# Optimization experiments

Hardware: AMD Instinct MI355X
Metric: run time of the kernel (lower is better)

## Reference

```python
import jax, jax.numpy as jnp
import numpy as np

E = 192      # embed_dim
DI = 384     # d_inner = 2*E (mamba default expand=2)
S = 16       # d_state
R = 12       # dt_rank = ceil(E/16)
DEPTH = 4
STRIDE = 4
P = 400      # num_patches = 1600/4
NC = 20
BATCH = 32
EPS = 1e-5


def _rmsnorm(x, w):
    x = x.astype(jnp.float32)
    return x * jax.lax.rsqrt(jnp.mean(x * x, axis=-1, keepdims=True) + EPS) * w


def _mamba_mixer(h, in_w, cw, cb, xpw, dtw, dtb, a_log, d_skip, ow):
    # h: [B, L, E]
    Bsz, Ln, _ = h.shape
    xz = jnp.einsum('ble,de->bld', h, in_w)            # [B,L,2*DI]
    xm, z = xz[..., :DI], xz[..., DI:]
    # causal depthwise conv1d, kernel 4 (left pad 3, truncate to L)
    xp = jnp.pad(xm, ((0, 0), (3, 0), (0, 0)))
    xc = sum(xp[:, k:k + Ln, :] * cw[:, k] for k in range(4)) + cb
    xc = jax.nn.silu(xc)
    xdb = jnp.einsum('bld,rd->blr', xc, xpw)           # [B,L,R+2S]
    dt = jax.nn.softplus(jnp.einsum('blr,dr->bld', xdb[..., :R], dtw) + dtb)
    Bm = xdb[..., R:R + S]
    Cm = xdb[..., R + S:]
    A = -jnp.exp(a_log)                                # [DI,S]

    def step(hst, inp):
        dt_t, b_t, c_t, u_t = inp                      # [B,DI],[B,S],[B,S],[B,DI]
        dA = jnp.exp(dt_t[:, :, None] * A)             # [B,DI,S]
        hst = dA * hst + (dt_t * u_t)[:, :, None] * b_t[:, None, :]
        y_t = jnp.einsum('bdn,bn->bd', hst, c_t)
        return hst, y_t

    h0 = jnp.zeros((Bsz, DI, S), xc.dtype)
    xs = (dt.transpose(1, 0, 2), Bm.transpose(1, 0, 2), Cm.transpose(1, 0, 2), xc.transpose(1, 0, 2))
    _, ys = jax.lax.scan(step, h0, xs)
    y = ys.transpose(1, 0, 2) + xc * d_skip
    y = y * jax.nn.silu(z)
    return jnp.einsum('bld,ed->ble', y, ow)


def _forward(imgs, patch_w, patch_b, cls_token, pos_embed, cnn_w, cnn_b, norm_w,
             in_proj_w, conv_w, conv_b, x_proj_w, dt_proj_w, dt_proj_b, A_log, D,
             out_proj_w, norm_f_w, head_w, head_b):
    Bsz = imgs.shape[0]
    # StrideEmbed: conv1d kernel=stride=4 == reshape + matmul
    x = imgs.reshape(Bsz, P, STRIDE)
    x = jnp.einsum('blk,ek->ble', x, patch_w[:, 0, :]) + patch_b   # [B,P,E]
    x = x + pos_embed[:, :-1, :]
    # depthwise conv1d k=3 pad=1 over length
    xp = jnp.pad(x, ((0, 0), (1, 1), (0, 0)))
    x = sum(xp[:, k:k + P, :] * cnn_w[:, 0, k] for k in range(3)) + cnn_b
    cls = cls_token + pos_embed[:, -1, :]                           # [1,1,E]
    x = jnp.concatenate([x, jnp.broadcast_to(cls, (Bsz, 1, E))], axis=1)  # [B,401,E]

    hidden = x
    residual = None
    for i in range(DEPTH):
        residual = hidden if residual is None else residual + hidden
        hn = _rmsnorm(residual, norm_w[i])
        hidden = _mamba_mixer(hn, in_proj_w[i], conv_w[i], conv_b[i], x_proj_w[i],
                              dt_proj_w[i], dt_proj_b[i], A_log[i], D[i], out_proj_w[i])
    out = _rmsnorm(hidden + residual, norm_f_w)
    v_sem = out[:, -1, :]
    return v_sem @ head_w.T + head_b


def setup_inputs() -> dict:
    key = jax.random.key(0)
    ks = jax.random.split(key, 12)
    n = lambda k, shp, s=0.02: jax.random.normal(k, shp, dtype=jnp.float32) * s
    return {
        'imgs': jax.random.normal(ks[0], (BATCH, 1, 40, 40), jnp.float32),
        'patch_w': n(ks[1], (E, 1, STRIDE), 0.3),
        'patch_b': jnp.zeros((E,), jnp.float32),
        'cls_token': n(ks[2], (1, 1, E)),
        'pos_embed': n(ks[3], (1, P + 1, E)),
        'cnn_w': n(ks[4], (E, 1, 3), 0.3),
        'cnn_b': jnp.zeros((E,), jnp.float32),
        'norm_w': jnp.ones((DEPTH, E), jnp.float32),
        'in_proj_w': n(ks[5], (DEPTH, 2 * DI, E), 0.05),
        'conv_w': n(ks[6], (DEPTH, DI, 4), 0.3),
        'conv_b': jnp.zeros((DEPTH, DI), jnp.float32),
        'x_proj_w': n(ks[7], (DEPTH, R + 2 * S, DI), 0.05),
        'dt_proj_w': n(ks[8], (DEPTH, DI, R), 0.3),
        'dt_proj_b': jnp.log(jnp.expm1(jax.random.uniform(ks[9], (DEPTH, DI), minval=0.001, maxval=0.1))),
        'A_log': jnp.log(jnp.broadcast_to(jnp.arange(1, S + 1, dtype=jnp.float32), (DEPTH, DI, S))),
        'D': jnp.ones((DEPTH, DI), jnp.float32),
        'out_proj_w': n(ks[10], (DEPTH, E, DI), 0.05),
        'norm_f_w': jnp.ones((E,), jnp.float32),
        'head_w': n(ks[11], (NC, E)),
        'head_b': jnp.zeros((NC,), jnp.float32),
    }


def reference(imgs, patch_w, patch_b, cls_token, pos_embed, cnn_w, cnn_b, norm_w,
              in_proj_w, conv_w, conv_b, x_proj_w, dt_proj_w, dt_proj_b, A_log, D,
              out_proj_w, norm_f_w, head_w, head_b):
    return _forward(imgs, patch_w, patch_b, cls_token, pos_embed, cnn_w, cnn_b, norm_w,
                    in_proj_w, conv_w, conv_b, x_proj_w, dt_proj_w, dt_proj_b, A_log, D,
                    out_proj_w, norm_f_w, head_w, head_b)
```

## Files before the change

kernel.cpp:

```cpp
#include <hip/hip_runtime.h>
#include <math.h>

#define E 192
#define DI 384
#define S 16
#define R 12
#define DEPTH 4
#define P 400
#define NC 20
#define BATCH 32
#define L 401
#define NTOK (BATCH * L)
#define CH 32
#define NCH 13

using short8 = __attribute__((ext_vector_type(8))) short;
using float4v = __attribute__((ext_vector_type(4))) float;

__device__ __forceinline__ float siluf(float x) {
    return x / (1.f + __expf(-x));
}
__device__ __forceinline__ float softplusf(float x) {
    return (x > 20.f) ? x : log1pf(__expf(x));
}
__device__ __forceinline__ unsigned short f2bf(float x) {
    unsigned int u = __float_as_uint(x);
    unsigned int r = 0x7fffu + ((u >> 16) & 1u);
    return (unsigned short)((u + r) >> 16);
}
__device__ __forceinline__ float bf2f(unsigned short v) {
    return __uint_as_float(((unsigned int)v) << 16);
}

__global__ void k_embed(const float* __restrict__ imgs, const float* __restrict__ patch_w,
                        const float* __restrict__ patch_b, const float* __restrict__ cls_token,
                        const float* __restrict__ pos_embed, const float* __restrict__ cnn_w,
                        const float* __restrict__ cnn_b, float* __restrict__ resid) {
    int idx = blockIdx.x * blockDim.x + threadIdx.x;
    if (idx >= NTOK * E) return;
    int e = idx % E;
    int bl = idx / E;
    int l = bl % L;
    int b = bl / L;
    float out;
    if (l == P) {
        out = cls_token[e] + pos_embed[(size_t)P * E + e];
    } else {
        float w0 = patch_w[e * 4 + 0], w1 = patch_w[e * 4 + 1];
        float w2 = patch_w[e * 4 + 2], w3 = patch_w[e * 4 + 3];
        float pb = patch_b[e];
        const float* ib = imgs + (size_t)b * 1600;
        auto xe = [&](int ll) -> float {
            const float* ip = ib + ll * 4;
            return ip[0] * w0 + ip[1] * w1 + ip[2] * w2 + ip[3] * w3 + pb +
                   pos_embed[(size_t)ll * E + e];
        };
        float c0 = cnn_w[e * 3 + 0], c1 = cnn_w[e * 3 + 1], c2 = cnn_w[e * 3 + 2];
        float acc = cnn_b[e] + xe(l) * c1;
        if (l > 0) acc += xe(l - 1) * c0;
        if (l < P - 1) acc += xe(l + 1) * c2;
        out = acc;
    }
    resid[idx] = out;
}

__global__ void k_rmsnorm(const float* __restrict__ resid, unsigned short* __restrict__ hn,
                          const float* __restrict__ w) {
    int wave = blockIdx.x * (blockDim.x >> 6) + (threadIdx.x >> 6);
    int lane = threadIdx.x & 63;
    if (wave >= NTOK) return;
    size_t base = (size_t)wave * E;
    float v[3];
    float ss = 0.f;
#pragma unroll
    for (int j = 0; j < 3; j++) {
        int e = lane + j * 64;
        float r = resid[base + e];
        v[j] = r;
        ss += r * r;
    }
#pragma unroll
    for (int off = 32; off > 0; off >>= 1) ss += __shfl_xor(ss, off, 64);
    float scale = rsqrtf(ss * (1.f / (float)E) + 1e-5f);
#pragma unroll
    for (int j = 0; j < 3; j++) {
        int e = lane + j * 64;
        hn[base + e] = f2bf(v[j] * scale * w[e]);
    }
}

__global__ void k_prep(const float* __restrict__ in_proj_w, const float* __restrict__ x_proj_w,
                       const float* __restrict__ out_proj_w, const float* __restrict__ A_log,
                       const float* __restrict__ dt_proj_w,
                       unsigned short* __restrict__ w_in, unsigned short* __restrict__ w_x,
                       unsigned short* __restrict__ w_out, float* __restrict__ negA,
                       float* __restrict__ dtw_t) {
    const int n1 = DEPTH * 2 * DI * E;
    const int n2 = DEPTH * 44 * DI;
    const int n3 = DEPTH * E * DI;
    const int n4 = DEPTH * DI * S;
    const int n5 = DEPTH * DI * R;
    int idx = blockIdx.x * blockDim.x + threadIdx.x;
    if (idx < n1) {
        w_in[idx] = f2bf(in_proj_w[idx]);
    } else if (idx < n1 + n2) {
        int i = idx - n1;
        w_x[i] = f2bf(x_proj_w[i]);
    } else if (idx < n1 + n2 + n3) {
        int i = idx - n1 - n2;
        w_out[i] = f2bf(out_proj_w[i]);
    } else if (idx < n1 + n2 + n3 + n4) {
        int i = idx - n1 - n2 - n3;
        int layer = i / (DI * S);
        int rem = i % (DI * S);
        int n = rem / DI;
        int d = rem % DI;
        negA[i] = -__expf(A_log[(size_t)layer * DI * S + d * S + n]);
    } else if (idx < n1 + n2 + n3 + n4 + n5) {
        int i = idx - n1 - n2 - n3 - n4;
        int layer = i / (DI * R);
        int rem = i % (DI * R);
        int r = rem / DI;
        int d = rem % DI;
        dtw_t[i] = dt_proj_w[(size_t)layer * DI * R + d * R + r];
    }
}

__global__ void k_flag(const float* __restrict__ negA, int* __restrict__ flag) {
    int idx = blockIdx.x * blockDim.x + threadIdx.x;
    if (idx >= DEPTH * DI) return;
    int layer = idx / DI;
    int d = idx % DI;
    const float* base = negA + (size_t)layer * DI * S;
    float a0 = base[d];
    bool ok = true;
#pragma unroll
    for (int n = 1; n < S; n++) {
        float an = base[n * DI + d];
        ok = ok && (fabsf(an - (float)(n + 1) * a0) <= 1e-5f * fabsf(an));
    }
    flag[idx] = ok ? 1 : 0;
}

template <int BM, int BN, int EPI>
__global__ __launch_bounds__(256) void k_gemm_bf16(const unsigned short* __restrict__ A,
                                                   const unsigned short* __restrict__ W,
                                                   float* __restrict__ C,
                                                   unsigned short* __restrict__ XM,
                                                   unsigned short* __restrict__ Z,
                                                   int M, int N, int K) {
    constexpr int BK = 64, PADK = BK + 8;
    constexpr int MT = BM / 32, NT = BN / 32;
    __shared__ unsigned short As[BM][PADK];
    __shared__ unsigned short Bs[BN][PADK];
    int tid = threadIdx.x;
    int m0 = blockIdx.y * BM, n0 = blockIdx.x * BN;
    int wave = tid >> 6, lane = tid & 63;
    int row16 = lane & 15, quad = lane >> 4;
    int wm0 = (wave >> 1) * (BM / 2), wn0 = (wave & 1) * (BN / 2);

    float4v acc[MT][NT];
#pragma unroll
    for (int i = 0; i < MT; i++)
#pragma unroll
        for (int j = 0; j < NT; j++) acc[i][j] = (float4v){0.f, 0.f, 0.f, 0.f};

    for (int k0 = 0; k0 < K; k0 += BK) {
#pragma unroll
        for (int p = 0; p < MT; p++) {
            int idx = (p * 256 + tid) * 8;
            int row = idx / BK, col = idx % BK;
            int gm = m0 + row;
            short8 v;
            if (gm < M)
                v = *(const short8*)&A[(size_t)gm * K + k0 + col];
            else
                v = (short8)0;
            *(short8*)&As[row][col] = v;
        }
#pragma unroll
        for (int p = 0; p < NT; p++) {
            int idx = (p * 256 + tid) * 8;
            int row = idx / BK, col = idx % BK;
            int gn = n0 + row;
            short8 v;
            if (gn < N)
                v = *(const short8*)&W[(size_t)gn * K + k0 + col];
            else
                v = (short8)0;
            *(short8*)&Bs[row][col] = v;
        }
        __syncthreads();
#pragma unroll
        for (int kk = 0; kk < BK; kk += 32) {
            int koff = kk + quad * 8;
            short8 af[MT], bfr[NT];
#pragma unroll
            for (int i = 0; i < MT; i++)
                af[i] = *(const short8*)&As[wm0 + i * 16 + row16][koff];
#pragma unroll
            for (int j = 0; j < NT; j++)
                bfr[j] = *(const short8*)&Bs[wn0 + j * 16 + row16][koff];
#pragma unroll
            for (int i = 0; i < MT; i++)
#pragma unroll
                for (int j = 0; j < NT; j++)
                    acc[i][j] = __builtin_amdgcn_mfma_f32_16x16x32_bf16(af[i], bfr[j],
                                                                        acc[i][j], 0, 0, 0);
        }
        __syncthreads();
    }
#pragma unroll
    for (int i = 0; i < MT; i++) {
#pragma unroll
        for (int j = 0; j < NT; j++) {
#pragma unroll
            for (int r = 0; r < 4; r++) {
                int m = m0 + wm0 + i * 16 + quad * 4 + r;
                int n = n0 + wn0 + j * 16 + row16;
                if (m >= M || n >= N) continue;
                float v = acc[i][j][r];
                if (EPI == 0) {
                    C[(size_t)m * N + n] = v;
                } else if (EPI == 1) {
                    if (n < DI)
                        XM[(size_t)m * DI + n] = f2bf(v);
                    else
                        Z[(size_t)m * DI + (n - DI)] = f2bf(v);
                } else {
                    C[(size_t)m * N + n] += v;
                }
            }
        }
    }
}

__global__ void k_conv(const unsigned short* __restrict__ xm_bf, const float* __restrict__ cw,
                       const float* __restrict__ cb, unsigned short* __restrict__ xc_bf) {
    int idx = blockIdx.x * blockDim.x + threadIdx.x;
    if (idx >= NTOK * DI) return;
    int d = idx % DI;
    int bl = idx / DI;
    int l = bl % L;
    int b = bl / L;
    const unsigned short* base = xm_bf + (size_t)b * L * DI + d;
    float acc = cb[d];
#pragma unroll
    for (int k = 0; k < 4; k++) {
        int ll = l - 3 + k;
        if (ll >= 0) acc += bf2f(base[(size_t)ll * DI]) * cw[d * 4 + k];
    }
    xc_bf[idx] = f2bf(siluf(acc));
}

__global__ __launch_bounds__(384) void k_dtpre(
        const float* __restrict__ xdb, const float* __restrict__ dtw_t,
        const float* __restrict__ dtb, float* __restrict__ dtbuf) {
    int tok = blockIdx.x;
    int d = threadIdx.x;
    const float* xr = xdb + (size_t)tok * 44;
    float acc = dtb[d];
#pragma unroll
    for (int r = 0; r < R; r++) acc += xr[r] * dtw_t[r * DI + d];
    dtbuf[(size_t)tok * DI + d] = softplusf(acc);
}

template <bool LAST>
__global__ __launch_bounds__(384) void k_scanA(
        const unsigned short* __restrict__ xc_bf, const float* __restrict__ xdb,
        const float* __restrict__ dtbuf, const float* __restrict__ negA_l,
        const int* __restrict__ flag_l, const float* __restrict__ Dskip,
        float2* __restrict__ ydt, float* __restrict__ hend) {
    int d = threadIdx.x;
    int ch = blockIdx.x;
    int b = blockIdx.y;
    int t0 = ch * CH;
    int t1 = min(t0 + CH, L);
    bool fast = __all(flag_l[d] != 0);
    float a0 = negA_l[d];
    float a[S];
    if (!fast) {
#pragma unroll
        for (int n = 0; n < S; n++) a[n] = negA_l[n * DI + d];
    }
    float dsk = Dskip[d];
    float h[S] = {};
    float dts = 0.f;
    size_t tok0 = (size_t)b * L + t0;
    float dt_nx = dtbuf[tok0 * DI + d];
    float u_nx = bf2f(xc_bf[tok0 * DI + d]);
    float e1_nx = __expf(a0 * dt_nx);
    for (int t = t0; t < t1; t++) {
        size_t tok = (size_t)b * L + t;
        float dtv = dt_nx, e1v = e1_nx, uu = u_nx;
        if (t + 1 < t1) {
            dt_nx = dtbuf[(tok + 1) * DI + d];
            u_nx = bf2f(xc_bf[(tok + 1) * DI + d]);
            e1_nx = __expf(a0 * dt_nx);
        }
        const float* row = xdb + tok * 44;
        dts += dtv;
        float dtu = dtv * uu;
        float y = uu * dsk;
        if (fast) {
            float p = e1v;
#pragma unroll
            for (int n = 0; n < S; n++) {
                h[n] = p * h[n] + dtu * row[R + n];
                y += h[n] * row[R + S + n];
                p *= e1v;
            }
        } else {
#pragma unroll
            for (int n = 0; n < S; n++) {
                float dA = __expf(dtv * a[n]);
                h[n] = dA * h[n] + dtu * row[R + n];
                y += h[n] * row[R + S + n];
            }
        }
        if (!LAST || t == P || t == t1 - 1) ydt[tok * DI + d] = make_float2(y, dts);
    }
    float* he = hend + ((size_t)(b * NCH + ch) * S) * DI + d;
#pragma unroll
    for (int n = 0; n < S; n++) he[n * DI] = h[n];
}

__global__ void k_scanB(const float* __restrict__ hend, const float2* __restrict__ ydt,
                        const float* __restrict__ negA_l, const int* __restrict__ flag_l,
                        float* __restrict__ hinit) {
    int idx = blockIdx.x * blockDim.x + threadIdx.x;
    if (idx >= BATCH * DI) return;
    int d = idx % DI;
    int b = idx / DI;
    bool fast = __all(flag_l[d] != 0);
    float a[S];
#pragma unroll
    for (int n = 0; n < S; n++) a[n] = negA_l[n * DI + d];
    float h[S] = {};
    for (int ch = 0; ch < NCH; ch++) {
        size_t o = ((size_t)(b * NCH + ch) * S) * DI + d;
#pragma unroll
        for (int n = 0; n < S; n++) hinit[o + n * DI] = h[n];
        int tlast = min(ch * CH + CH, L) - 1;
        float dts = ydt[((size_t)b * L + tlast) * DI + d].y;
        if (fast) {
            float e1c = __expf(a[0] * dts);
            float p = e1c;
#pragma unroll
            for (int n = 0; n < S; n++) {
                h[n] = p * h[n] + hend[o + n * DI];
                p *= e1c;
            }
        } else {
#pragma unroll
            for (int n = 0; n < S; n++) h[n] = __expf(dts * a[n]) * h[n] + hend[o + n * DI];
        }
    }
}

__global__ __launch_bounds__(384) void k_fixup(
        const unsigned short* __restrict__ z_bf, const float* __restrict__ xdb,
        const float* __restrict__ negA_l, const int* __restrict__ flag_l,
        const float* __restrict__ hinit, const float2* __restrict__ ydt,
        unsigned short* __restrict__ y_bf) {
    int tok = blockIdx.x;
    int d = threadIdx.x;
    int l = tok % L;
    int b = tok / L;
    int ch = l / CH;
    size_t idx = (size_t)tok * DI + d;
    float2 yd = ydt[idx];
    float y = yd.x;
    if (ch != 0) {
        bool fast = __all(flag_l[d] != 0);
        const float* h0 = hinit + ((size_t)(b * NCH + ch) * S) * DI + d;
        const float* cv = xdb + (size_t)tok * 44 + R + S;
        float dts = yd.y;
        float corr = 0.f;
        if (fast) {
            float e1c = __expf(negA_l[d] * dts);
            float p = e1c;
#pragma unroll
            for (int n = 0; n < S; n++) {
                corr += cv[n] * p * h0[n * DI];
                p *= e1c;
            }
        } else {
#pragma unroll
            for (int n = 0; n < S; n++)
                corr += cv[n] * __expf(negA_l[n * DI + d] * dts) * h0[n * DI];
        }
        y += corr;
    }
    float z = bf2f(z_bf[idx]);
    y_bf[idx] = f2bf(y * siluf(z));
}

__global__ __launch_bounds__(384) void k_fixup_last(
        const unsigned short* __restrict__ z_bf, const float* __restrict__ xdb,
        const float* __restrict__ negA_l, const int* __restrict__ flag_l,
        const float* __restrict__ hinit, const float2* __restrict__ ydt,
        unsigned short* __restrict__ y32) {
    int b = blockIdx.x;
    int d = threadIdx.x;
    int tok = b * L + P;
    int ch = P / CH;
    size_t idx = (size_t)tok * DI + d;
    float2 yd = ydt[idx];
    float y = yd.x;
    {
        bool fast = __all(flag_l[d] != 0);
        const float* h0 = hinit + ((size_t)(b * NCH + ch) * S) * DI + d;
        const float* cv = xdb + (size_t)tok * 44 + R + S;
        float dts = yd.y;
        float corr = 0.f;
        if (fast) {
            float e1c = __expf(negA_l[d] * dts);
            float p = e1c;
#pragma unroll
            for (int n = 0; n < S; n++) {
                corr += cv[n] * p * h0[n * DI];
                p *= e1c;
            }
        } else {
#pragma unroll
            for (int n = 0; n < S; n++)
                corr += cv[n] * __expf(negA_l[n * DI + d] * dts) * h0[n * DI];
        }
        y += corr;
    }
    float z = bf2f(z_bf[idx]);
    y32[(size_t)b * DI + d] = f2bf(y * siluf(z));
}

__global__ void k_head(const float* __restrict__ resid, const float* __restrict__ hidden32,
                       const float* __restrict__ norm_f_w, const float* __restrict__ head_w,
                       const float* __restrict__ head_b, float* __restrict__ out) {
    __shared__ float v[E];
    int b = blockIdx.x;
    int lane = threadIdx.x;
    size_t base = ((size_t)b * L + P) * E;
    float loc[3];
    float ss = 0.f;
#pragma unroll
    for (int j = 0; j < 3; j++) {
        int e = lane + j * 64;
        float x = resid[base + e] + hidden32[(size_t)b * E + e];
        loc[j] = x;
        ss += x * x;
    }
#pragma unroll
    for (int off = 32; off > 0; off >>= 1) ss += __shfl_xor(ss, off, 64);
    float scale = rsqrtf(ss * (1.f / (float)E) + 1e-5f);
#pragma unroll
    for (int j = 0; j < 3; j++) {
        int e = lane + j * 64;
        v[e] = loc[j] * scale * norm_f_w[e];
    }
    __syncthreads();
    if (lane < NC) {
        float acc = head_b[lane];
        for (int e = 0; e < E; e++) acc += v[e] * head_w[lane * E + e];
        out[b * NC + lane] = acc;
    }
}

extern "C" void kernel_launch(void* const* d_in, const int* in_sizes, int n_in,
                              void* d_out, int out_size, void* d_ws, size_t ws_size,
                              hipStream_t stream) {
    const float* imgs      = (const float*)d_in[0];
    const float* patch_w   = (const float*)d_in[1];
    const float* patch_b   = (const float*)d_in[2];
    const float* cls_token = (const float*)d_in[3];
    const float* pos_embed = (const float*)d_in[4];
    const float* cnn_w     = (const float*)d_in[5];
    const float* cnn_b     = (const float*)d_in[6];
    const float* norm_w    = (const float*)d_in[7];
    const float* in_proj_w = (const float*)d_in[8];
    const float* conv_w    = (const float*)d_in[9];
    const float* conv_b    = (const float*)d_in[10];
    const float* x_proj_w  = (const float*)d_in[11];
    const float* dt_proj_w = (const float*)d_in[12];
    const float* dt_proj_b = (const float*)d_in[13];
    const float* A_log     = (const float*)d_in[14];
    const float* Dskip     = (const float*)d_in[15];
    const float* out_proj_w= (const float*)d_in[16];
    const float* norm_f_w  = (const float*)d_in[17];
    const float* head_w    = (const float*)d_in[18];
    const float* head_b    = (const float*)d_in[19];

    float* ws = (float*)d_ws;
    size_t off = 0;
    float* resid  = ws + off; off += (size_t)NTOK * E;
    float* xdb    = ws + off; off += (size_t)NTOK * 44;
    float* dtbuf  = ws + off; off += (size_t)NTOK * DI;
    float* ydt    = ws + off; off += (size_t)NTOK * DI * 2;
    float* hend   = ws + off; off += (size_t)BATCH * NCH * DI * S;
    float* hinit  = ws + off; off += (size_t)BATCH * NCH * DI * S;
    float* negA   = ws + off; off += (size_t)DEPTH * DI * S;
    float* dtw_t  = ws + off; off += (size_t)DEPTH * DI * R;
    float* hid32  = ws + off; off += (size_t)BATCH * E;
    int*   gflag  = (int*)(ws + off); off += (size_t)DEPTH * DI;
    unsigned short* xm_bf  = (unsigned short*)(ws + off); off += (size_t)NTOK * DI / 2;
    unsigned short* z_bf   = (unsigned short*)(ws + off); off += (size_t)NTOK * DI / 2;
    unsigned short* bf_buf = (unsigned short*)(ws + off); off += (size_t)NTOK * DI / 2;
    unsigned short* y32_bf = (unsigned short*)(ws + off); off += (size_t)BATCH * DI / 2 + 16;
    unsigned short* w_in  = (unsigned short*)(ws + off); off += (size_t)DEPTH * 2 * DI * E / 2;
    unsigned short* w_x   = (unsigned short*)(ws + off); off += (size_t)DEPTH * 44 * DI / 2 + 16;
    unsigned short* w_out = (unsigned short*)(ws + off); off += (size_t)DEPTH * E * DI / 2;

    unsigned short* hn_bf = bf_buf;
    unsigned short* xc_bf = bf_buf;
    unsigned short* y_bf  = bf_buf;

    {
        int ntot = DEPTH * (2 * DI * E + 44 * DI + E * DI + DI * S + DI * R);
        k_prep<<<(ntot + 255) / 256, 256, 0, stream>>>(in_proj_w, x_proj_w, out_proj_w, A_log,
                                                       dt_proj_w, w_in, w_x, w_out, negA,
                                                       dtw_t);
        k_flag<<<(DEPTH * DI + 255) / 256, 256, 0, stream>>>(negA, gflag);
    }

    k_embed<<<(NTOK * E) / 256, 256, 0, stream>>>(imgs, patch_w, patch_b, cls_token,
                                                  pos_embed, cnn_w, cnn_b, resid);

    for (int i = 0; i < DEPTH; i++) {
        k_rmsnorm<<<NTOK / 4, 256, 0, stream>>>(resid, hn_bf, norm_w + i * E);

        {
            dim3 g((2 * DI) / 64, (NTOK + 127) / 128);
            k_gemm_bf16<128, 64, 1><<<g, 256, 0, stream>>>(
                hn_bf, w_in + (size_t)i * 2 * DI * E, nullptr, xm_bf, z_bf, NTOK, 2 * DI, E);
        }
        k_conv<<<(NTOK * DI) / 256, 256, 0, stream>>>(xm_bf, conv_w + (size_t)i * DI * 4,
                                                      conv_b + (size_t)i * DI, xc_bf);
        {
            dim3 g(1, NTOK / 32);
            k_gemm_bf16<32, 64, 0><<<g, 256, 0, stream>>>(
                xc_bf, w_x + (size_t)i * 44 * DI, xdb, nullptr, nullptr, NTOK, 44, DI);
        }
        const float* nA = negA + (size_t)i * DI * S;
        const int* fl = gflag + (size_t)i * DI;
        k_dtpre<<<NTOK, 384, 0, stream>>>(xdb, dtw_t + (size_t)i * DI * R,
                                          dt_proj_b + (size_t)i * DI, dtbuf);
        dim3 g(NCH, BATCH);
        if (i < DEPTH - 1) {
            k_scanA<false><<<g, DI, 0, stream>>>(xc_bf, xdb, dtbuf, nA, fl,
                                                 Dskip + (size_t)i * DI, (float2*)ydt, hend);
            k_scanB<<<(BATCH * DI + 255) / 256, 256, 0, stream>>>(hend, (const float2*)ydt,
                                                                  nA, fl, hinit);
            k_fixup<<<NTOK, 384, 0, stream>>>(z_bf, xdb, nA, fl, hinit,
                                              (const float2*)ydt, y_bf);
            dim3 go(E / 64, (NTOK + 63) / 64);
            k_gemm_bf16<64, 64, 2><<<go, 256, 0, stream>>>(
                y_bf, w_out + (size_t)i * E * DI, resid, nullptr, nullptr, NTOK, E, DI);
        } else {
            k_scanA<true><<<g, DI, 0, stream>>>(xc_bf, xdb, dtbuf, nA, fl,
                                                Dskip + (size_t)i * DI, (float2*)ydt, hend);
            k_scanB<<<(BATCH * DI + 255) / 256, 256, 0, stream>>>(hend, (const float2*)ydt,
                                                                  nA, fl, hinit);
            k_fixup_last<<<BATCH, 384, 0, stream>>>(z_bf, xdb, nA, fl, hinit,
                                                    (const float2*)ydt, y32_bf);
            dim3 go(E / 64, 1);
            k_gemm_bf16<32, 64, 0><<<go, 256, 0, stream>>>(
                y32_bf, w_out + (size_t)i * E * DI, hid32, nullptr, nullptr, BATCH, E, DI);
        }
    }

    k_head<<<BATCH, 64, 0, stream>>>(resid, hid32, norm_f_w, head_w, head_b, (float*)d_out);
}
```

Measured before the change: 731.1 us.

## Fuse causal depthwise conv into x_proj GEMM and retile in/out projections

Removes the standalone depthwise conv kernel and computes conv+SiLU while loading A tiles in a new x_proj GEMM kernel, still writing xc_bf for the scan. This saves one launch and a separate read of xm plus the reread of xc. The in_proj GEMM tile grows to 128x128 and the out_proj GEMM tile to 128x64. The trade-offs are that each xm element is loaded four times inside the fused kernel, and the larger tiles give fewer blocks per launch.

```diff
diff --git a/kernel.cpp b/kernel.cpp
--- a/kernel.cpp
+++ b/kernel.cpp
@@ -235,22 +235,100 @@
     }
 }
 
-__global__ void k_conv(const unsigned short* __restrict__ xm_bf, const float* __restrict__ cw,
-                       const float* __restrict__ cb, unsigned short* __restrict__ xc_bf) {
-    int idx = blockIdx.x * blockDim.x + threadIdx.x;
-    if (idx >= NTOK * DI) return;
-    int d = idx % DI;
-    int bl = idx / DI;
-    int l = bl % L;
-    int b = bl / L;
-    const unsigned short* base = xm_bf + (size_t)b * L * DI + d;
-    float acc = cb[d];
-#pragma unroll
-    for (int k = 0; k < 4; k++) {
-        int ll = l - 3 + k;
-        if (ll >= 0) acc += bf2f(base[(size_t)ll * DI]) * cw[d * 4 + k];
-    }
-    xc_bf[idx] = f2bf(siluf(acc));
+template <int BM, int BN>
+__global__ __launch_bounds__(256) void k_xproj_conv(
+        const unsigned short* __restrict__ xm, const unsigned short* __restrict__ W,
+        const float* __restrict__ cw, const float* __restrict__ cb,
+        float* __restrict__ C, unsigned short* __restrict__ xc_bf, int M, int N) {
+    constexpr int K = DI, BK = 64, PADK = BK + 8;
+    constexpr int MT = BM / 32, NT = BN / 32;
+    __shared__ unsigned short As[BM][PADK];
+    __shared__ unsigned short Bs[BN][PADK];
+    int tid = threadIdx.x;
+    int m0 = blockIdx.y * BM;
+    int wave = tid >> 6, lane = tid & 63;
+    int row16 = lane & 15, quad = lane >> 4;
+    int wm0 = (wave >> 1) * (BM / 2), wn0 = (wave & 1) * (BN / 2);
+
+    float4v acc[MT][NT];
+#pragma unroll
+    for (int i = 0; i < MT; i++)
+#pragma unroll
+        for (int j = 0; j < NT; j++) acc[i][j] = (float4v){0.f, 0.f, 0.f, 0.f};
+
+    for (int k0 = 0; k0 < K; k0 += BK) {
+#pragma unroll
+        for (int p = 0; p < MT; p++) {
+            int idx = (p * 256 + tid) * 8;
+            int row = idx / BK, col = idx % BK;
+            int t = m0 + row;
+            short8 v = (short8)0;
+            if (t < M) {
+                int l = t % L;
+                int d0 = k0 + col;
+                float av[8];
+#pragma unroll
+                for (int j = 0; j < 8; j++) av[j] = cb[d0 + j];
+#pragma unroll
+                for (int k = 0; k < 4; k++) {
+                    int ll = l - 3 + k;
+                    if (ll >= 0) {
+                        short8 xv = *(const short8*)&xm[(size_t)(t - 3 + k) * DI + d0];
+#pragma unroll
+                        for (int j = 0; j < 8; j++)
+                            av[j] += bf2f((unsigned short)xv[j]) * cw[(d0 + j) * 4 + k];
+                    }
+                }
+#pragma unroll
+                for (int j = 0; j < 8; j++) v[j] = (short)f2bf(siluf(av[j]));
+                *(short8*)&xc_bf[(size_t)t * DI + d0] = v;
+            }
+            *(short8*)&As[row][col] = v;
+        }
+#pragma unroll
+        for (int p = 0; p < NT; p++) {
+            int idx = (p * 256 + tid) * 8;
+            int row = idx / BK, col = idx % BK;
+            short8 v;
+            if (row < N)
+                v = *(const short8*)&W[(size_t)row * K + k0 + col];
+            else
+                v = (short8)0;
+            *(short8*)&Bs[row][col] = v;
+        }
+        __syncthreads();
+#pragma unroll
+        for (int kk = 0; kk < BK; kk += 32) {
+            int koff = kk + quad * 8;
+            short8 af[MT], bfr[NT];
+#pragma unroll
+            for (int i = 0; i < MT; i++)
+                af[i] = *(const short8*)&As[wm0 + i * 16 + row16][koff];
+#pragma unroll
+            for (int j = 0; j < NT; j++)
+                bfr[j] = *(const short8*)&Bs[wn0 + j * 16 + row16][koff];
+#pragma unroll
+            for (int i = 0; i < MT; i++)
+#pragma unroll
+                for (int j = 0; j < NT; j++)
+                    acc[i][j] = __builtin_amdgcn_mfma_f32_16x16x32_bf16(af[i], bfr[j],
+                                                                        acc[i][j], 0, 0, 0);
+        }
+        __syncthreads();
+    }
+#pragma unroll
+    for (int i = 0; i < MT; i++) {
+#pragma unroll
+        for (int j = 0; j < NT; j++) {
+#pragma unroll
+            for (int r = 0; r < 4; r++) {
+                int m = m0 + wm0 + i * 16 + quad * 4 + r;
+                int n = wn0 + j * 16 + row16;
+                if (m >= M || n >= N) continue;
+                C[(size_t)m * N + n] = acc[i][j][r];
+            }
+        }
+    }
 }
 
 __global__ __launch_bounds__(384) void k_dtpre(
@@ -528,16 +606,15 @@
         k_rmsnorm<<<NTOK / 4, 256, 0, stream>>>(resid, hn_bf, norm_w + i * E);
 
         {
-            dim3 g((2 * DI) / 64, (NTOK + 127) / 128);
-            k_gemm_bf16<128, 64, 1><<<g, 256, 0, stream>>>(
+            dim3 g((2 * DI) / 128, (NTOK + 127) / 128);
+            k_gemm_bf16<128, 128, 1><<<g, 256, 0, stream>>>(
                 hn_bf, w_in + (size_t)i * 2 * DI * E, nullptr, xm_bf, z_bf, NTOK, 2 * DI, E);
         }
-        k_conv<<<(NTOK * DI) / 256, 256, 0, stream>>>(xm_bf, conv_w + (size_t)i * DI * 4,
-                                                      conv_b + (size_t)i * DI, xc_bf);
         {
-            dim3 g(1, NTOK / 32);
-            k_gemm_bf16<32, 64, 0><<<g, 256, 0, stream>>>(
-                xc_bf, w_x + (size_t)i * 44 * DI, xdb, nullptr, nullptr, NTOK, 44, DI);
+            dim3 g(1, (NTOK + 63) / 64);
+            k_xproj_conv<64, 64><<<g, 256, 0, stream>>>(
+                xm_bf, w_x + (size_t)i * 44 * DI, conv_w + (size_t)i * DI * 4,
+                conv_b + (size_t)i * DI, xdb, xc_bf, NTOK, 44);
         }
         const float* nA = negA + (size_t)i * DI * S;
         const int* fl = gflag + (size_t)i * DI;
@@ -551,8 +628,8 @@
                                                                   nA, fl, hinit);
             k_fixup<<<NTOK, 384, 0, stream>>>(z_bf, xdb, nA, fl, hinit,
                                               (const float2*)ydt, y_bf);
-            dim3 go(E / 64, (NTOK + 63) / 64);
-            k_gemm_bf16<64, 64, 2><<<go, 256, 0, stream>>>(
+            dim3 go(E / 64, (NTOK + 127) / 128);
+            k_gemm_bf16<128, 64, 2><<<go, 256, 0, stream>>>(
                 y_bf, w_out + (size_t)i * E * DI, resid, nullptr, nullptr, NTOK, E, DI);
         } else {
             k_scanA<true><<<g, DI, 0, stream>>>(xc_bf, xdb, dtbuf, nA, fl,
```

Result: slower. 767.6 us (+5.0%).

## Fuse causal conv, x_proj GEMM and dt projection into one per-token kernel

Applied to the files above, without the earlier changes.

Replaces three launches (depthwise conv+silu, small x_proj MFMA GEMM, dt_proj+softplus) with a single kernel where each wavefront handles one token. The conv output is kept in shared memory for the 44-wide x_proj dot products, and the dt rank slice is reused from shared memory for the dt projection. This removes two launches and the global round trips of xc and xdb between stages. The cost is that x_proj becomes scalar FMAs on 44 of 64 lanes instead of matrix-core work, and each block reloads the x_proj weights.

```diff
diff --git a/kernel.cpp b/kernel.cpp
--- a/kernel.cpp
+++ b/kernel.cpp
@@ -13,6 +13,7 @@
 #define NTOK (BATCH * L)
 #define CH 32
 #define NCH 13
+#define XTOKS 6
 
 using short8 = __attribute__((ext_vector_type(8))) short;
 using float4v = __attribute__((ext_vector_type(4))) float;
@@ -235,34 +236,55 @@
     }
 }
 
-__global__ void k_conv(const unsigned short* __restrict__ xm_bf, const float* __restrict__ cw,
-                       const float* __restrict__ cb, unsigned short* __restrict__ xc_bf) {
-    int idx = blockIdx.x * blockDim.x + threadIdx.x;
-    if (idx >= NTOK * DI) return;
-    int d = idx % DI;
-    int bl = idx / DI;
-    int l = bl % L;
-    int b = bl / L;
-    const unsigned short* base = xm_bf + (size_t)b * L * DI + d;
-    float acc = cb[d];
-#pragma unroll
-    for (int k = 0; k < 4; k++) {
-        int ll = l - 3 + k;
-        if (ll >= 0) acc += bf2f(base[(size_t)ll * DI]) * cw[d * 4 + k];
-    }
-    xc_bf[idx] = f2bf(siluf(acc));
-}
-
-__global__ __launch_bounds__(384) void k_dtpre(
-        const float* __restrict__ xdb, const float* __restrict__ dtw_t,
-        const float* __restrict__ dtb, float* __restrict__ dtbuf) {
-    int tok = blockIdx.x;
-    int d = threadIdx.x;
-    const float* xr = xdb + (size_t)tok * 44;
-    float acc = dtb[d];
-#pragma unroll
-    for (int r = 0; r < R; r++) acc += xr[r] * dtw_t[r * DI + d];
-    dtbuf[(size_t)tok * DI + d] = softplusf(acc);
+__global__ __launch_bounds__(XTOKS * 64) void k_xall(
+        const unsigned short* __restrict__ xm_bf, const float* __restrict__ cw,
+        const float* __restrict__ cb, const unsigned short* __restrict__ w_x,
+        const float* __restrict__ dtw_t, const float* __restrict__ dtb,
+        unsigned short* __restrict__ xc_bf, float* __restrict__ xdb,
+        float* __restrict__ dtbuf) {
+    __shared__ float xs[XTOKS][DI];
+    __shared__ float xd[XTOKS][44];
+    int wv = threadIdx.x >> 6;
+    int lane = threadIdx.x & 63;
+    int tok = blockIdx.x * XTOKS + wv;
+    if (tok >= NTOK) return;
+    int l = tok % L;
+#pragma unroll
+    for (int j = 0; j < DI / 64; j++) {
+        int d = lane + 64 * j;
+        float acc = cb[d];
+#pragma unroll
+        for (int k = 0; k < 4; k++) {
+            int ll = l - 3 + k;
+            if (ll >= 0)
+                acc += bf2f(xm_bf[(size_t)(tok - 3 + k) * DI + d]) * cw[d * 4 + k];
+        }
+        unsigned short us = f2bf(siluf(acc));
+        xc_bf[(size_t)tok * DI + d] = us;
+        xs[wv][d] = bf2f(us);
+    }
+    if (lane < 44) {
+        const unsigned short* wr = w_x + (size_t)lane * DI;
+        float acc = 0.f;
+#pragma unroll 4
+        for (int kk = 0; kk < DI; kk += 8) {
+            short8 w8 = *(const short8*)&wr[kk];
+            const float* xp = &xs[wv][kk];
+#pragma unroll
+            for (int j = 0; j < 8; j++)
+                acc += xp[j] * bf2f((unsigned short)w8[j]);
+        }
+        xdb[(size_t)tok * 44 + lane] = acc;
+        xd[wv][lane] = acc;
+    }
+#pragma unroll
+    for (int j = 0; j < DI / 64; j++) {
+        int d = lane + 64 * j;
+        float a2 = dtb[d];
+#pragma unroll
+        for (int r = 0; r < R; r++) a2 += xd[wv][r] * dtw_t[r * DI + d];
+        dtbuf[(size_t)tok * DI + d] = softplusf(a2);
+    }
 }
 
 template <bool LAST>
@@ -532,17 +554,15 @@
             k_gemm_bf16<128, 64, 1><<<g, 256, 0, stream>>>(
                 hn_bf, w_in + (size_t)i * 2 * DI * E, nullptr, xm_bf, z_bf, NTOK, 2 * DI, E);
         }
-        k_conv<<<(NTOK * DI) / 256, 256, 0, stream>>>(xm_bf, conv_w + (size_t)i * DI * 4,
-                                                      conv_b + (size_t)i * DI, xc_bf);
         {
-            dim3 g(1, NTOK / 32);
-            k_gemm_bf16<32, 64, 0><<<g, 256, 0, stream>>>(
-                xc_bf, w_x + (size_t)i * 44 * DI, xdb, nullptr, nullptr, NTOK, 44, DI);
+            int g = (NTOK + XTOKS - 1) / XTOKS;
+            k_xall<<<g, XTOKS * 64, 0, stream>>>(
+                xm_bf, conv_w + (size_t)i * DI * 4, conv_b + (size_t)i * DI,
+                w_x + (size_t)i * 44 * DI, dtw_t + (size_t)i * DI * R,
+                dt_proj_b + (size_t)i * DI, xc_bf, xdb, dtbuf);
         }
         const float* nA = negA + (size_t)i * DI * S;
         const int* fl = gflag + (size_t)i * DI;
-        k_dtpre<<<NTOK, 384, 0, stream>>>(xdb, dtw_t + (size_t)i * DI * R,
-                                          dt_proj_b + (size_t)i * DI, dtbuf);
         dim3 g(NCH, BATCH);
         if (i < DEPTH - 1) {
             k_scanA<false><<<g, DI, 0, stream>>>(xc_bf, xdb, dtbuf, nA, fl,
```

Result: slower. 896.8 us (+22.7%).
